# Optimization experiments

Hardware: AMD Instinct MI355X
Metric: run time of the kernel (lower is better)

Reference implementation:

```python
import jax, jax.numpy as jnp
import numpy as np

B, W, F, D, H, L = 8, 256, 16, 128, 8, 4
DH = D                      # dim_head = embedding_dims in the original call
INNER = H * DH              # 1024
TIME_EMB = 4
SCALE = DH ** -0.5


def causal_conv(x, w, b, dilation):
    # x: [B, F, W]; w: [F, 1, K] depthwise (groups=F); left-pad (K-1)*dilation -> causal
    k = w.shape[-1]
    pad = (k - 1) * dilation
    y = jax.lax.conv_general_dilated(
        x, w, window_strides=(1,), padding=[(pad, 0)], rhs_dilation=(dilation,),
        dimension_numbers=("NCH", "OIH", "NCH"), feature_group_count=F)
    return y + b[None, :, None]


def sinusoidal_pe(length, d):
    pos = jnp.arange(length, dtype=jnp.float32)[:, None]
    div = jnp.exp(jnp.arange(0, d, 2, dtype=jnp.float32) * (-np.log(10000.0) / d))
    pe = jnp.zeros((length, d), dtype=jnp.float32)
    pe = pe.at[:, 0::2].set(jnp.sin(pos * div)).at[:, 1::2].set(jnp.cos(pos * div))
    return pe  # [W, D]


def layer_norm(x, g, b):
    m = x.mean(-1, keepdims=True)
    v = x.var(-1, keepdims=True)
    return (x - m) * jax.lax.rsqrt(v + 1e-5) * g + b


def vt_attention(x, g, bln, wqkv, wout, bout):
    # x: [B, W, F, D] -> PreNorm then dual-axis (variable + temporal) attention
    h = layer_norm(x, g, bln)
    qkv = h @ wqkv                                   # [B,W,F,3*INNER]
    q, k, v = jnp.split(qkv, 3, axis=-1)
    heads = lambda t: t.reshape(B, W, F, H, DH)
    q, k, v = heads(q) * SCALE, heads(k), heads(v)
    # variable attention: attend across the feature axis (per time step)
    av = jax.nn.softmax(jnp.einsum("bwihe,bwjhe->bwhij", q, k), axis=-1)  # [B,W,H,F,F]
    ov = jnp.einsum("bwhij,bwjhe->bwihe", av, v)
    # temporal attention: attend across the window axis (per variable)
    at = jax.nn.softmax(jnp.einsum("bifhe,bjfhe->bfhij", q, k), axis=-1)  # [B,F,H,W,W]
    ot = jnp.einsum("bfhij,bjfhe->bifhe", at, v)
    o = (ov + ot).reshape(B, W, F, INNER)
    return o @ wout + bout                            # [B,W,F,D]


def setup_inputs() -> dict:
    key = jax.random.key(0)
    ks = jax.random.split(key, 16)
    n = lambda k, shape, sc: jax.random.normal(k, shape, dtype=jnp.float32) * sc
    return {
        "x": jax.random.normal(ks[0], (B, W, F), dtype=jnp.float32),
        "conv_w1": n(ks[1], (F, 1, 4), 0.3), "conv_b1": jnp.zeros((F,), jnp.float32),
        "conv_w2": n(ks[2], (F, 1, 8), 0.2), "conv_b2": jnp.zeros((F,), jnp.float32),
        "conv_w3": n(ks[3], (F, 1, 16), 0.15), "conv_b3": jnp.zeros((F,), jnp.float32),
        "w_val": n(ks[4], (TIME_EMB, D), 0.3), "b_val": jnp.zeros((D,), jnp.float32),
        "ln_g": jnp.ones((L, D), jnp.float32), "ln_b": jnp.zeros((L, D), jnp.float32),
        "w_qkv": n(ks[5], (L, D, 3 * INNER), D ** -0.5),
        "w_out": n(ks[6], (L, INNER, D), INNER ** -0.5),
        "b_out": jnp.zeros((L, D), jnp.float32),
        "w_head": n(ks[7], (F * D, F), (F * D) ** -0.5),
        "b_head": jnp.zeros((F,), jnp.float32),
    }


def reference(x, conv_w1, conv_b1, conv_w2, conv_b2, conv_w3, conv_b3,
              w_val, b_val, ln_g, ln_b, w_qkv, w_out, b_out, w_head, b_head):
    xt = jnp.transpose(x, (0, 2, 1))                  # b w f -> b f w
    c1 = causal_conv(xt, conv_w1, conv_b1, 1)
    c2 = causal_conv(xt, conv_w2, conv_b2, 2)
    c3 = causal_conv(xt, conv_w3, conv_b3, 3)
    s = jnp.stack([xt, c1, c2, c3], axis=-1)          # [B,F,W,4]
    s = jnp.transpose(s, (0, 2, 1, 3))                # [B,W,F,4]
    e = s @ w_val + b_val                             # [B,W,F,D]
    pe = sinusoidal_pe(W, D)                          # [W,D] broadcast over b,f
    h = e + pe[None, :, None, :]
    for l in range(L):
        xo = vt_attention(h, ln_g[l], ln_b[l], w_qkv[l], w_out[l], b_out[l])
        h = xo + h                                    # residual
    out = h.reshape(B, W, F * D) @ w_head + b_head    # [B,W,F]
    return out
```

## Files before the change

kernel.cpp:

```cpp
#include <hip/hip_runtime.h>
#include <hip/hip_bf16.h>
#include <math.h>

#define BB 8
#define WW 256
#define FF 16
#define DD 128
#define HH 8
#define NTOK (BB*WW*FF)
#define QSCALE 0.12751745f
#define INV_D (1.0f/128.0f)
#define LN10K_D 0.07195578415606394f

typedef __hip_bfloat16 bf16;
typedef short bf16x8 __attribute__((ext_vector_type(8)));
typedef float f32x4 __attribute__((ext_vector_type(4)));

__device__ __forceinline__ float bf2f(bf16 x){ return __bfloat162float(x); }
__device__ __forceinline__ bf16 f2bf(float x){ return __float2bfloat16(x); }
__device__ __forceinline__ unsigned short bfbits(float x){ bf16 b = f2bf(x); return *(unsigned short*)&b; }
__device__ __forceinline__ float bits2f(unsigned short u){ bf16 b = *(bf16*)&u; return __bfloat162float(b); }

#define MFMA16 __builtin_amdgcn_mfma_f32_16x16x32_bf16


__global__ __launch_bounds__(256) void prep_kernel(
    const float* __restrict__ wqkv, const float* __restrict__ wout,
    const float* __restrict__ wh,
    bf16* __restrict__ wqkvT, bf16* __restrict__ woutT, bf16* __restrict__ whT,
    const float* __restrict__ x,
    const float* __restrict__ w1, const float* __restrict__ b1,
    const float* __restrict__ w2, const float* __restrict__ b2,
    const float* __restrict__ w3, const float* __restrict__ b3,
    const float* __restrict__ wval, const float* __restrict__ bval,
    const float* __restrict__ g, const float* __restrict__ bln,
    float* __restrict__ h, bf16* __restrict__ hn)
{
    __shared__ __align__(16) char smem[16640];
    int tid = threadIdx.x;

    if (blockIdx.x < 544) {
        float (*tile)[65] = (float(*)[65])smem;
        int bx = blockIdx.x;
        const float* in; bf16* outp; int r0, c0, sin, sout, nmax;
        if (bx < 384) {
            int l = bx / 96, t = bx % 96;
            r0 = (t / 48)*64; c0 = (t % 48)*64;
            in = wqkv + (size_t)l*128*3072; outp = wqkvT + (size_t)l*3072*128;
            sin = 3072; sout = 128; nmax = 3072;
        } else if (bx < 512) {
            int j = bx - 384, l = j / 32, t = j % 32;
            r0 = (t / 2)*64; c0 = (t % 2)*64;
            in = wout + (size_t)l*1024*128; outp = woutT + (size_t)l*128*1024;
            sin = 128; sout = 1024; nmax = 128;
        } else {
            int t = bx - 512;
            r0 = t*64; c0 = 0;
            in = wh; outp = whT; sin = 16; sout = 2048; nmax = 16;
        }
        int rr = tid >> 2, cg = (tid & 3)*16;
        if (c0 + cg < nmax) {
            const float* src = in + (size_t)(r0 + rr)*sin + c0 + cg;
            #pragma unroll
            for (int i = 0; i < 4; i++)
                *(float4*)&tile[rr][cg + i*4] = *(const float4*)(src + i*4);
        }
        __syncthreads();
        int n = c0 + rr;
        if (n < nmax) {
            union { uint4 u[2]; unsigned short sh[16]; } o;
            #pragma unroll
            for (int e = 0; e < 16; e++) o.sh[e] = bfbits(tile[cg + e][rr]);
            bf16* dst = outp + (size_t)n*sout + r0 + cg;
            *(uint4*)dst = o.u[0];
            *(uint4*)(dst + 8) = o.u[1];
        }
        return;
    }

    float (*s)[4] = (float(*)[4])smem;
    float* hs = (float*)(smem + 256);
    int bw = blockIdx.x - 544;
    int b = bw >> 8, w = bw & 255;
    if (tid < 64) {
        int f = tid >> 2, t = tid & 3;
        const float* xb = x + (size_t)b*WW*FF + f;
        float v;
        if (t == 0) {
            v = xb[(size_t)w*FF];
        } else if (t == 1) {
            float acc = b1[f];
            #pragma unroll
            for (int kk = 0; kk < 4; kk++) { int t0 = w - (3-kk); if (t0 >= 0) acc += w1[f*4+kk]*xb[(size_t)t0*FF]; }
            v = acc;
        } else if (t == 2) {
            float acc = b2[f];
            #pragma unroll
            for (int kk = 0; kk < 8; kk++) { int t0 = w - (7-kk)*2; if (t0 >= 0) acc += w2[f*8+kk]*xb[(size_t)t0*FF]; }
            v = acc;
        } else {
            float acc = b3[f];
            #pragma unroll
            for (int kk = 0; kk < 16; kk++) { int t0 = w - (15-kk)*3; if (t0 >= 0) acc += w3[f*16+kk]*xb[(size_t)t0*FF]; }
            v = acc;
        }
        s[f][t] = v;
    }
    __syncthreads();
    #pragma unroll
    for (int r = 0; r < 8; r++) {
        int lin = r*256 + tid;
        int f = lin >> 7, d = lin & 127;
        float div = expf(-(float)(d & ~1) * LN10K_D);
        float arg = (float)w * div;
        float pe = (d & 1) ? cosf(arg) : sinf(arg);
        float e = bval[d] + pe;
        #pragma unroll
        for (int t = 0; t < 4; t++) e += s[f][t]*wval[t*128 + d];
        h[((size_t)bw*FF + f)*128 + d] = e;
        hs[f*132 + d] = e;
    }
    __syncthreads();
    int tok = tid >> 4, sub = tid & 15;
    float xv[8];
    #pragma unroll
    for (int e2 = 0; e2 < 8; e2++) xv[e2] = hs[tok*132 + sub*8 + e2];
    float s1 = 0.f, s2 = 0.f;
    #pragma unroll
    for (int e2 = 0; e2 < 8; e2++) { s1 += xv[e2]; s2 += xv[e2]*xv[e2]; }
    #pragma unroll
    for (int m = 1; m < 16; m <<= 1) { s1 += __shfl_xor(s1, m, 64); s2 += __shfl_xor(s2, m, 64); }
    float mean = s1*INV_D;
    float var  = s2*INV_D - mean*mean;
    float rs = rsqrtf(var + 1e-5f);
    union { uint4 u; unsigned short sh[8]; } ou;
    #pragma unroll
    for (int e2 = 0; e2 < 8; e2++) {
        int d = sub*8 + e2;
        ou.sh[e2] = bfbits((xv[e2]-mean)*rs*g[d] + bln[d]);
    }
    *(uint4*)(hn + ((size_t)bw*16 + tok)*128 + sub*8) = ou.u;
}

__global__ __launch_bounds__(256) void qkv_mfma(
    const bf16* __restrict__ hn, const bf16* __restrict__ wT,
    bf16* __restrict__ q, bf16* __restrict__ k, bf16* __restrict__ v)
{
    __shared__ __align__(16) unsigned short Cs[4][64][72];
    int tid = threadIdx.x;
    int lane = tid & 63, wave = tid >> 6;
    int quad = lane >> 4, l16 = lane & 15;
    int wm = wave >> 1, wn = wave & 1;
    int m0 = blockIdx.x * 128, n0 = blockIdx.y * 128;

    f32x4 acc[4][4];
    #pragma unroll
    for (int a = 0; a < 4; a++)
        #pragma unroll
        for (int c = 0; c < 4; c++) acc[a][c] = 0.f;

    #pragma unroll
    for (int kt = 0; kt < 4; kt++) {
        int ko = kt*32 + quad*8;
        bf16x8 af[4], bfr[4];
        #pragma unroll
        for (int tm = 0; tm < 4; tm++)
            af[tm] = *(const bf16x8*)(hn + (size_t)(m0 + wm*64 + tm*16 + l16)*128 + ko);
        #pragma unroll
        for (int tn = 0; tn < 4; tn++)
            bfr[tn] = *(const bf16x8*)(wT + (size_t)(n0 + wn*64 + tn*16 + l16)*128 + ko);
        #pragma unroll
        for (int tm = 0; tm < 4; tm++)
            #pragma unroll
            for (int tn = 0; tn < 4; tn++)
                acc[tm][tn] = MFMA16(af[tm], bfr[tn], acc[tm][tn], 0, 0, 0);
    }

    bf16* dst; int nrel; float scl; int isq;
    if (n0 < 1024)      { dst = q; nrel = n0;        scl = QSCALE; isq = 1; }
    else if (n0 < 2048) { dst = k; nrel = n0 - 1024; scl = 1.0f;   isq = 0; }
    else                { dst = v; nrel = n0 - 2048; scl = 1.0f;   isq = 0; }

    #pragma unroll
    for (int tm = 0; tm < 4; tm++)
        #pragma unroll
        for (int tn = 0; tn < 4; tn++)
            #pragma unroll
            for (int r = 0; r < 4; r++)
                Cs[wave][tm*16 + quad*4 + r][tn*16 + l16] = bfbits(acc[tm][tn][r]*scl);

    if (isq) {
        #pragma unroll
        for (int p = 0; p < 8; p++) {
            int row = p*8 + (lane >> 3);
            int c8  = (lane & 7)*8;
            uint4 val = *(const uint4*)&Cs[wave][row][c8];
            size_t gaddr = (size_t)(m0 + wm*64 + row)*1024 + nrel + wn*64 + c8;
            *(uint4*)(dst + gaddr) = val;
        }
    } else {
        int hh = nrel >> 7;
        #pragma unroll
        for (int p = 0; p < 8; p++) {
            int row = p*8 + (lane >> 3);
            int c8  = (lane & 7)*8;
            uint4 val = *(const uint4*)&Cs[wave][row][c8];
            int tok = m0 + wm*64 + row;
            int bl = tok >> 12, w = (tok >> 4) & 255, f = tok & 15;
            int d  = wn*64 + c8;
            size_t gaddr = ((size_t)((bl*16 + f)*8 + hh) << 15) + (size_t)w*128 + d;
            *(uint4*)(dst + gaddr) = val;
        }
    }
}

__global__ __launch_bounds__(256) void tattn_mfma(
    const bf16* __restrict__ q, const bf16* __restrict__ k, const bf16* __restrict__ v,
    bf16* __restrict__ o)
{
    __shared__ __align__(16) unsigned short Ks[64*136];
    __shared__ __align__(16) unsigned short VsT[128*72];
    __shared__ __align__(16) unsigned short Ps[4][16][72];
    unsigned short* Os = Ks;
    unsigned int* VsTdw = (unsigned int*)VsT;

    int bx = blockIdx.x;
    int hh = bx & 7, it2 = (bx>>3) & 1, f = (bx>>4) & 15, bl = bx >> 8;
    int tid = threadIdx.x;
    int lane = tid & 63, wave = tid >> 6;
    int quad = lane >> 4, l16 = lane & 15;

    size_t baseQ = ((size_t)(bl*WW)*FF + f)*1024 + (size_t)hh*128;
    size_t baseK = (size_t)((bl*16 + f)*8 + hh) << 15;

    #pragma unroll 1
    for (int pass = 0; pass < 2; pass++) {
        int i0 = it2*128 + pass*64;

        bf16x8 af[4];
        {
            size_t qa = baseQ + (size_t)(i0 + wave*16 + l16)*16384;
            #pragma unroll
            for (int kt = 0; kt < 4; kt++)
                af[kt] = *(const bf16x8*)(q + qa + kt*32 + quad*8);
        }

        f32x4 oacc[8];
        #pragma unroll
        for (int t = 0; t < 8; t++) oacc[t] = 0.f;
        float m_run[4], l_run[4];
        #pragma unroll
        for (int r = 0; r < 4; r++) { m_run[r] = -1e30f; l_run[r] = 0.f; }

        #pragma unroll 1
        for (int jt = 0; jt < 4; jt++) {
            __syncthreads();
            #pragma unroll
            for (int p4 = 0; p4 < 4; p4++) {
                int lin = p4*256 + tid;
                int row = lin >> 4, c8 = (lin & 15)*8;
                uint4 kv = *(const uint4*)(k + baseK + (size_t)(jt*64 + row)*128 + c8);
                *(uint4*)&Ks[row*136 + c8] = kv;
            }
            #pragma unroll
            for (int p = 0; p < 2; p++) {
                int lin = p*256 + tid;
                int j2 = lin & 31;
                int c2 = (lin >> 5)*8;
                union { uint4 u; unsigned short sh[8]; } a, b;
                a.u = *(const uint4*)(v + baseK + (size_t)(jt*64 + 2*j2)*128 + c2);
                b.u = *(const uint4*)(v + baseK + (size_t)(jt*64 + 2*j2 + 1)*128 + c2);
                int col2 = (((2*j2) + (c2 & 56)) & 63) >> 1;
                #pragma unroll
                for (int e = 0; e < 8; e++)
                    VsTdw[(c2+e)*36 + col2] = (unsigned int)a.sh[e] | ((unsigned int)b.sh[e] << 16);
            }
            __syncthreads();

            f32x4 st[4];
            #pragma unroll
            for (int t = 0; t < 4; t++) st[t] = 0.f;
            #pragma unroll
            for (int t = 0; t < 4; t++) {
                #pragma unroll
                for (int kt = 0; kt < 4; kt++) {
                    bf16x8 kf = *(const bf16x8*)&Ks[(t*16 + l16)*136 + kt*32 + quad*8];
                    st[t] = MFMA16(af[kt], kf, st[t], 0, 0, 0);
                }
            }

            float tmax[4];
            #pragma unroll
            for (int r = 0; r < 4; r++) tmax[r] = fmaxf(fmaxf(st[0][r], st[1][r]), fmaxf(st[2][r], st[3][r]));
            #pragma unroll
            for (int m = 1; m < 16; m <<= 1)
                #pragma unroll
                for (int r = 0; r < 4; r++) tmax[r] = fmaxf(tmax[r], __shfl_xor(tmax[r], m, 64));
            float alpha[4], rsum[4];
            #pragma unroll
            for (int r = 0; r < 4; r++) {
                float mnew = fmaxf(m_run[r], tmax[r]);
                alpha[r] = exp2f(m_run[r] - mnew);
                m_run[r] = mnew;
                rsum[r] = 0.f;
            }
            #pragma unroll
            for (int t = 0; t < 4; t++)
                #pragma unroll
                for (int r = 0; r < 4; r++) {
                    float pp = exp2f(st[t][r] - m_run[r]);
                    st[t][r] = pp;
                    rsum[r] += pp;
                }
            #pragma unroll
            for (int m = 1; m < 16; m <<= 1)
                #pragma unroll
                for (int r = 0; r < 4; r++) rsum[r] += __shfl_xor(rsum[r], m, 64);
            #pragma unroll
            for (int r = 0; r < 4; r++) l_run[r] = l_run[r]*alpha[r] + rsum[r];
            #pragma unroll
            for (int t = 0; t < 8; t++)
                #pragma unroll
                for (int r = 0; r < 4; r++) oacc[t][r] *= alpha[r];

            #pragma unroll
            for (int t = 0; t < 4; t++)
                #pragma unroll
                for (int r = 0; r < 4; r++)
                    Ps[wave][quad*4+r][t*16+l16] = bfbits(st[t][r]);

            #pragma unroll
            for (int kt2 = 0; kt2 < 2; kt2++) {
                int kbase = kt2*32 + quad*8;
                bf16x8 pf = *(const bf16x8*)&Ps[wave][l16][kbase];
                #pragma unroll
                for (int t = 0; t < 8; t++) {
                    int d = t*16 + l16;
                    int colstart = (kbase + (((d>>3)&7) << 3)) & 63;
                    bf16x8 vf = *(const bf16x8*)&VsT[d*72 + colstart];
                    oacc[t] = MFMA16(pf, vf, oacc[t], 0, 0, 0);
                }
            }
        }

        __syncthreads();
        float inv[4];
        #pragma unroll
        for (int r = 0; r < 4; r++) inv[r] = 1.f / l_run[r];
        #pragma unroll
        for (int t = 0; t < 8; t++)
            #pragma unroll
            for (int r = 0; r < 4; r++)
                Os[(wave*16 + quad*4 + r)*136 + t*16 + l16] = bfbits(oacc[t][r]*inv[r]);
        __syncthreads();
        #pragma unroll
        for (int r4 = 0; r4 < 4; r4++) {
            int row = r4*4 + quad;
            uint4 val = *(const uint4*)&Os[(wave*16 + row)*136 + l16*8];
            size_t gaddr = baseQ + (size_t)(i0 + wave*16 + row)*16384 + l16*8;
            *(uint4*)(o + gaddr) = val;
        }
    }
}

__global__ __launch_bounds__(256) void vproj_mfma(
    const bf16* __restrict__ q, const bf16* __restrict__ k, const bf16* __restrict__ v,
    const bf16* __restrict__ ot, const bf16* __restrict__ woT,
    const float* __restrict__ bo, float* __restrict__ h,
    bf16* __restrict__ hn, const float* __restrict__ gN, const float* __restrict__ bN,
    int donorm, int tokbase)
{
    __shared__ __align__(16) unsigned short VsT[16768];
    __shared__ __align__(16) unsigned short Ps[4][16][24];
    __shared__ float red2[4][16][2];
    unsigned short* Osum = VsT;
    unsigned int* VsTdw = (unsigned int*)VsT;

    int tid = threadIdx.x;
    int lane = tid & 63, wave = tid >> 6, quad = lane >> 4, l16 = lane & 15;
    int bl = blockIdx.x >> 8, w = blockIdx.x & 255;
    size_t base = (size_t)blockIdx.x * 16384;
    size_t woff = (size_t)w * 128;

    uint4 otpre[8];
    #pragma unroll
    for (int u = 0; u < 8; u++) {
        int lin = u*256 + tid;
        int fr = lin >> 7, dc = (lin & 127)*8;
        otpre[u] = *(const uint4*)(ot + base + (size_t)fr*1024 + dc);
    }

    #pragma unroll
    for (int p = 0; p < 4; p++) {
        int lin = p*256 + tid;
        int j2 = lin & 7;
        int d0 = (lin >> 3)*8;
        int hh2 = d0 >> 7, dd = d0 & 127;
        union { uint4 u; unsigned short sh[8]; } a, b;
        a.u = *(const uint4*)(v + (((size_t)((bl*16 + 2*j2  )*8 + hh2)) << 15) + woff + dd);
        b.u = *(const uint4*)(v + (((size_t)((bl*16 + 2*j2+1)*8 + hh2)) << 15) + woff + dd);
        #pragma unroll
        for (int e = 0; e < 8; e++)
            VsTdw[(d0+e)*8 + j2] = (unsigned int)a.sh[e] | ((unsigned int)b.sh[e] << 16);
    }
    __syncthreads();

    bf16x8 zf = {0,0,0,0,0,0,0,0};
    f32x4 oa[2][8];
    #pragma unroll
    for (int hi = 0; hi < 2; hi++) {
        int hh = wave*2 + hi;
        size_t hb = base + hh*128;

        f32x4 s = {0.f,0.f,0.f,0.f};
        size_t ka = (((size_t)((bl*16 + l16)*8 + hh)) << 15) + woff;
        #pragma unroll
        for (int kt = 0; kt < 4; kt++) {
            bf16x8 qf = *(const bf16x8*)(q + hb + (size_t)l16*1024 + kt*32 + quad*8);
            bf16x8 kf = *(const bf16x8*)(k + ka + kt*32 + quad*8);
            s = MFMA16(qf, kf, s, 0, 0, 0);
        }
        float p[4];
        #pragma unroll
        for (int r = 0; r < 4; r++) {
            float mxv = s[r];
            #pragma unroll
            for (int m = 1; m < 16; m <<= 1) mxv = fmaxf(mxv, __shfl_xor(mxv, m, 64));
            float e = exp2f(s[r] - mxv);
            float smv = e;
            #pragma unroll
            for (int m = 1; m < 16; m <<= 1) smv += __shfl_xor(smv, m, 64);
            p[r] = e / smv;
        }
        #pragma unroll
        for (int r = 0; r < 4; r++) Ps[wave][quad*4+r][l16] = bfbits(p[r]);

        bf16x8 pf = zf;
        if (quad < 2) pf = *(const bf16x8*)&Ps[wave][l16][quad*8];
        #pragma unroll
        for (int dt = 0; dt < 8; dt++) oa[hi][dt] = 0.f;
        #pragma unroll
        for (int dt = 0; dt < 8; dt++) {
            bf16x8 vf = zf;
            if (quad < 2) vf = *(const bf16x8*)&VsT[(size_t)(hh*128 + dt*16 + l16)*16 + quad*8];
            oa[hi][dt] = MFMA16(pf, vf, oa[hi][dt], 0, 0, 0);
        }
    }

    __syncthreads();
    #pragma unroll
    for (int hi = 0; hi < 2; hi++) {
        int hh = wave*2 + hi;
        #pragma unroll
        for (int dt = 0; dt < 8; dt++)
            #pragma unroll
            for (int r = 0; r < 4; r++)
                Osum[(quad*4 + r)*1048 + hh*128 + dt*16 + l16] = bfbits(oa[hi][dt][r]);
    }
    __syncthreads();

    #pragma unroll
    for (int u = 0; u < 8; u++) {
        int lin = u*256 + tid;
        int fr = lin >> 7, dc = (lin & 127)*8;
        union { uint4 u4; unsigned short sh[8]; } a, bsh, wv;
        a.u4   = otpre[u];
        bsh.u4 = *(const uint4*)&Osum[fr*1048 + dc];
        #pragma unroll
        for (int e = 0; e < 8; e++)
            wv.sh[e] = bfbits(bits2f(a.sh[e]) + bits2f(bsh.sh[e]));
        *(uint4*)&Osum[fr*1048 + dc] = wv.u4;
    }
    __syncthreads();

    f32x4 pacc[2];
    pacc[0] = 0.f; pacc[1] = 0.f;
    #pragma unroll 4
    for (int kt2 = 0; kt2 < 32; kt2++) {
        bf16x8 af2 = *(const bf16x8*)&Osum[l16*1048 + kt2*32 + quad*8];
        #pragma unroll
        for (int nt = 0; nt < 2; nt++) {
            bf16x8 bfr = *(const bf16x8*)(woT + (size_t)(wave*32 + nt*16 + l16)*1024 + kt2*32 + quad*8);
            pacc[nt] = MFMA16(af2, bfr, pacc[nt], 0, 0, 0);
        }
    }

    int htok = tokbase + blockIdx.x*16;
    float hv[2][4];
    #pragma unroll
    for (int nt = 0; nt < 2; nt++) {
        int n = wave*32 + nt*16 + l16;
        float bias = bo[n];
        #pragma unroll
        for (int r = 0; r < 4; r++) {
            size_t idx = (size_t)(htok + quad*4 + r)*128 + n;
            float nv = h[idx] + pacc[nt][r] + bias;
            h[idx] = nv;
            hv[nt][r] = nv;
        }
    }

    if (donorm) {
        float s1[4], s2[4];
        #pragma unroll
        for (int r = 0; r < 4; r++) {
            s1[r] = hv[0][r] + hv[1][r];
            s2[r] = hv[0][r]*hv[0][r] + hv[1][r]*hv[1][r];
        }
        #pragma unroll
        for (int m = 1; m < 16; m <<= 1)
            #pragma unroll
            for (int r = 0; r < 4; r++) {
                s1[r] += __shfl_xor(s1[r], m, 64);
                s2[r] += __shfl_xor(s2[r], m, 64);
            }
        __syncthreads();
        if (l16 == 0) {
            #pragma unroll
            for (int r = 0; r < 4; r++) {
                red2[wave][quad*4+r][0] = s1[r];
                red2[wave][quad*4+r][1] = s2[r];
            }
        }
        __syncthreads();
        #pragma unroll
        for (int nt = 0; nt < 2; nt++) {
            int n = wave*32 + nt*16 + l16;
            float gn = gN[n], bn = bN[n];
            #pragma unroll
            for (int r = 0; r < 4; r++) {
                int t = quad*4 + r;
                float t1 = red2[0][t][0] + red2[1][t][0] + red2[2][t][0] + red2[3][t][0];
                float t2 = red2[0][t][1] + red2[1][t][1] + red2[2][t][1] + red2[3][t][1];
                float mean = t1*INV_D;
                float var  = t2*INV_D - mean*mean;
                float rsv = rsqrtf(var + 1e-5f);
                Osum[t*1048 + n] = bfbits((hv[nt][r]-mean)*rsv*gn + bn);
            }
        }
        __syncthreads();
        int row = tid >> 4, c8 = (tid & 15)*8;
        uint4 val = *(const uint4*)&Osum[row*1048 + c8];
        *(uint4*)(hn + (size_t)(htok + row)*128 + c8) = val;
    }
}

__global__ __launch_bounds__(256) void head_mfma(
    const float* __restrict__ h, const bf16* __restrict__ whT,
    const float* __restrict__ bh, float* __restrict__ out)
{
    __shared__ float sred[4][16][17];
    int tid = threadIdx.x;
    int lane = tid & 63, wave = tid >> 6, quad = lane >> 4, l16 = lane & 15;
    int bw0 = blockIdx.x * 16;
    const float* hrow = h + (size_t)(bw0 + l16)*2048 + wave*512;
    const bf16* wrow  = whT + (size_t)l16*2048 + wave*512;

    f32x4 acc = {0.f,0.f,0.f,0.f};
    #pragma unroll 4
    for (int kc = 0; kc < 16; kc++) {
        int ko = kc*32 + quad*8;
        float4 a0 = *(const float4*)(hrow + ko);
        float4 a1 = *(const float4*)(hrow + ko + 4);
        union { bf16x8 v; unsigned short sh[8]; } ua;
        ua.sh[0]=bfbits(a0.x); ua.sh[1]=bfbits(a0.y); ua.sh[2]=bfbits(a0.z); ua.sh[3]=bfbits(a0.w);
        ua.sh[4]=bfbits(a1.x); ua.sh[5]=bfbits(a1.y); ua.sh[6]=bfbits(a1.z); ua.sh[7]=bfbits(a1.w);
        bf16x8 bv = *(const bf16x8*)(wrow + ko);
        acc = MFMA16(ua.v, bv, acc, 0, 0, 0);
    }
    #pragma unroll
    for (int r = 0; r < 4; r++) sred[wave][quad*4+r][l16] = acc[r];
    __syncthreads();
    int i = tid >> 4, n = tid & 15;
    float s = bh[n] + sred[0][i][n] + sred[1][i][n] + sred[2][i][n] + sred[3][i][n];
    out[(size_t)(bw0 + i)*16 + n] = s;
}

extern "C" void kernel_launch(void* const* d_in, const int* in_sizes, int n_in,
                              void* d_out, int out_size, void* d_ws, size_t ws_size,
                              hipStream_t stream)
{
    const float* x    = (const float*)d_in[0];
    const float* w1   = (const float*)d_in[1];
    const float* b1   = (const float*)d_in[2];
    const float* w2   = (const float*)d_in[3];
    const float* b2   = (const float*)d_in[4];
    const float* w3   = (const float*)d_in[5];
    const float* b3   = (const float*)d_in[6];
    const float* wval = (const float*)d_in[7];
    const float* bval = (const float*)d_in[8];
    const float* lng  = (const float*)d_in[9];
    const float* lnb  = (const float*)d_in[10];
    const float* wqkv = (const float*)d_in[11];
    const float* wout = (const float*)d_in[12];
    const float* bout = (const float*)d_in[13];
    const float* wh   = (const float*)d_in[14];
    const float* bh   = (const float*)d_in[15];
    float* out = (float*)d_out;

    char* ws = (char*)d_ws;
    bf16*  wqkvT = (bf16*)ws;
    bf16*  woutT = (bf16*)(ws + 3145728);
    bf16*  whT   = (bf16*)(ws + 4194304);
    float* h     = (float*)(ws + 4259840);
    bf16*  hn    = (bf16*)(ws + 21037056);
    const size_t qoff = 29425664ull;

    int NBL = 1;
    if      (ws_size >= qoff + 8ull*4ull*8388608ull) NBL = 8;
    else if (ws_size >= qoff + 4ull*4ull*8388608ull) NBL = 4;
    else if (ws_size >= qoff + 2ull*4ull*8388608ull) NBL = 2;
    size_t bsz = (size_t)NBL * 8388608ull;
    bf16* q  = (bf16*)(ws + qoff);
    bf16* kk = (bf16*)(ws + qoff + bsz);
    bf16* vv = (bf16*)(ws + qoff + 2*bsz);
    bf16* oo = (bf16*)(ws + qoff + 3*bsz);

    prep_kernel<<<544 + BB*WW, 256, 0, stream>>>(
        wqkv, wout, wh, wqkvT, woutT, whT,
        x, w1,b1, w2,b2, w3,b3, wval, bval, lng, lnb, h, hn);

    for (int l = 0; l < 4; l++) {
        const bf16* wqT_l = wqkvT + (size_t)l*3072*128;
        const bf16* woT_l = woutT + (size_t)l*128*1024;
        const float* bo_l = bout + l*128;
        int donorm = (l < 3) ? 1 : 0;
        const float* gN = lng + (donorm ? (l+1)*128 : 0);
        const float* bN = lnb + (donorm ? (l+1)*128 : 0);
        for (int bb = 0; bb < BB; bb += NBL) {
            int tokbase = bb*WW*FF;
            qkv_mfma<<<dim3(NBL*32, 24), 256, 0, stream>>>(
                hn + (size_t)tokbase*128, wqT_l, q, kk, vv);
            tattn_mfma<<<NBL*FF*HH*2, 256, 0, stream>>>(q, kk, vv, oo);
            vproj_mfma<<<NBL*WW, 256, 0, stream>>>(q, kk, vv, oo, woT_l,
                                                   bo_l, h, hn, gN, bN,
                                                   donorm, tokbase);
        }
    }

    head_mfma<<<BB*WW/16, 256, 0, stream>>>(h, whT, bh, out);
}
```

Baseline: 1.447 ms.

## Split temporal attention blocks per 64-row tile, prefetch K/V into registers, hoist vproj loads

```diff
diff --git a/kernel.cpp b/kernel.cpp
--- a/kernel.cpp
+++ b/kernel.cpp
@@ -225,7 +225,8 @@
     unsigned int* VsTdw = (unsigned int*)VsT;
 
     int bx = blockIdx.x;
-    int hh = bx & 7, it2 = (bx>>3) & 1, f = (bx>>4) & 15, bl = bx >> 8;
+    int hh = bx & 7, it = (bx>>3) & 3, f = (bx>>5) & 15, bl = bx >> 9;
+    int i0 = it*64;
     int tid = threadIdx.x;
     int lane = tid & 63, wave = tid >> 6;
     int quad = lane >> 4, l16 = lane & 15;
@@ -233,133 +234,148 @@
     size_t baseQ = ((size_t)(bl*WW)*FF + f)*1024 + (size_t)hh*128;
     size_t baseK = (size_t)((bl*16 + f)*8 + hh) << 15;
 
+    bf16x8 af[4];
+    {
+        size_t qa = baseQ + (size_t)(i0 + wave*16 + l16)*16384;
+        #pragma unroll
+        for (int kt = 0; kt < 4; kt++)
+            af[kt] = *(const bf16x8*)(q + qa + kt*32 + quad*8);
+    }
+
+    f32x4 oacc[8];
+    #pragma unroll
+    for (int t = 0; t < 8; t++) oacc[t] = 0.f;
+    float m_run[4], l_run[4];
+    #pragma unroll
+    for (int r = 0; r < 4; r++) { m_run[r] = -1e30f; l_run[r] = 0.f; }
+
+    int krow = tid >> 4, kc8 = (tid & 15)*8;
+    int vj2 = tid & 31, vc2 = (tid >> 5)*8;
+
+    uint4 kld[4]; uint4 vla[2], vlb[2];
+    #pragma unroll
+    for (int p4 = 0; p4 < 4; p4++)
+        kld[p4] = *(const uint4*)(k + baseK + (size_t)(p4*16 + krow)*128 + kc8);
+    #pragma unroll
+    for (int p = 0; p < 2; p++) {
+        int j2 = vj2, c2 = p*128 + vc2;
+        j2 = (p*256 + tid) & 31; c2 = ((p*256 + tid) >> 5)*8;
+        vla[p] = *(const uint4*)(v + baseK + (size_t)(2*j2)*128 + c2);
+        vlb[p] = *(const uint4*)(v + baseK + (size_t)(2*j2 + 1)*128 + c2);
+    }
+
     #pragma unroll 1
-    for (int pass = 0; pass < 2; pass++) {
-        int i0 = it2*128 + pass*64;
-
-        bf16x8 af[4];
-        {
-            size_t qa = baseQ + (size_t)(i0 + wave*16 + l16)*16384;
-            #pragma unroll
-            for (int kt = 0; kt < 4; kt++)
-                af[kt] = *(const bf16x8*)(q + qa + kt*32 + quad*8);
-        }
-
-        f32x4 oacc[8];
-        #pragma unroll
-        for (int t = 0; t < 8; t++) oacc[t] = 0.f;
-        float m_run[4], l_run[4];
-        #pragma unroll
-        for (int r = 0; r < 4; r++) { m_run[r] = -1e30f; l_run[r] = 0.f; }
-
-        #pragma unroll 1
-        for (int jt = 0; jt < 4; jt++) {
-            __syncthreads();
-            #pragma unroll
-            for (int p4 = 0; p4 < 4; p4++) {
-                int lin = p4*256 + tid;
-                int row = lin >> 4, c8 = (lin & 15)*8;
-                uint4 kv = *(const uint4*)(k + baseK + (size_t)(jt*64 + row)*128 + c8);
-                *(uint4*)&Ks[row*136 + c8] = kv;
+    for (int jt = 0; jt < 4; jt++) {
+        __syncthreads();
+        #pragma unroll
+        for (int p4 = 0; p4 < 4; p4++)
+            *(uint4*)&Ks[(p4*16 + krow)*136 + kc8] = kld[p4];
+        #pragma unroll
+        for (int p = 0; p < 2; p++) {
+            int j2 = (p*256 + tid) & 31, c2 = ((p*256 + tid) >> 5)*8;
+            union { uint4 u; unsigned short sh[8]; } a, b;
+            a.u = vla[p]; b.u = vlb[p];
+            int col2 = (((2*j2) + (c2 & 56)) & 63) >> 1;
+            #pragma unroll
+            for (int e = 0; e < 8; e++)
+                VsTdw[(c2+e)*36 + col2] = (unsigned int)a.sh[e] | ((unsigned int)b.sh[e] << 16);
+        }
+        if (jt < 3) {
+            int jn = jt + 1;
+            #pragma unroll
+            for (int p4 = 0; p4 < 4; p4++)
+                kld[p4] = *(const uint4*)(k + baseK + (size_t)(jn*64 + p4*16 + krow)*128 + kc8);
+            #pragma unroll
+            for (int p = 0; p < 2; p++) {
+                int j2 = (p*256 + tid) & 31, c2 = ((p*256 + tid) >> 5)*8;
+                vla[p] = *(const uint4*)(v + baseK + (size_t)(jn*64 + 2*j2)*128 + c2);
+                vlb[p] = *(const uint4*)(v + baseK + (size_t)(jn*64 + 2*j2 + 1)*128 + c2);
             }
-            #pragma unroll
-            for (int p = 0; p < 2; p++) {
-                int lin = p*256 + tid;
-                int j2 = lin & 31;
-                int c2 = (lin >> 5)*8;
-                union { uint4 u; unsigned short sh[8]; } a, b;
-                a.u = *(const uint4*)(v + baseK + (size_t)(jt*64 + 2*j2)*128 + c2);
-                b.u = *(const uint4*)(v + baseK + (size_t)(jt*64 + 2*j2 + 1)*128 + c2);
-                int col2 = (((2*j2) + (c2 & 56)) & 63) >> 1;
-                #pragma unroll
-                for (int e = 0; e < 8; e++)
-                    VsTdw[(c2+e)*36 + col2] = (unsigned int)a.sh[e] | ((unsigned int)b.sh[e] << 16);
+        }
+        __syncthreads();
+
+        f32x4 st[4];
+        #pragma unroll
+        for (int t = 0; t < 4; t++) st[t] = 0.f;
+        #pragma unroll
+        for (int t = 0; t < 4; t++) {
+            #pragma unroll
+            for (int kt = 0; kt < 4; kt++) {
+                bf16x8 kf = *(const bf16x8*)&Ks[(t*16 + l16)*136 + kt*32 + quad*8];
+                st[t] = MFMA16(af[kt], kf, st[t], 0, 0, 0);
             }
-            __syncthreads();
-
-            f32x4 st[4];
-            #pragma unroll
-            for (int t = 0; t < 4; t++) st[t] = 0.f;
-            #pragma unroll
-            for (int t = 0; t < 4; t++) {
-                #pragma unroll
-                for (int kt = 0; kt < 4; kt++) {
-                    bf16x8 kf = *(const bf16x8*)&Ks[(t*16 + l16)*136 + kt*32 + quad*8];
-                    st[t] = MFMA16(af[kt], kf, st[t], 0, 0, 0);
-                }
+        }
+
+        float tmax[4];
+        #pragma unroll
+        for (int r = 0; r < 4; r++) tmax[r] = fmaxf(fmaxf(st[0][r], st[1][r]), fmaxf(st[2][r], st[3][r]));
+        #pragma unroll
+        for (int m = 1; m < 16; m <<= 1)
+            #pragma unroll
+            for (int r = 0; r < 4; r++) tmax[r] = fmaxf(tmax[r], __shfl_xor(tmax[r], m, 64));
+        float alpha[4], rsum[4];
+        #pragma unroll
+        for (int r = 0; r < 4; r++) {
+            float mnew = fmaxf(m_run[r], tmax[r]);
+            alpha[r] = exp2f(m_run[r] - mnew);
+            m_run[r] = mnew;
+            rsum[r] = 0.f;
+        }
+        #pragma unroll
+        for (int t = 0; t < 4; t++)
+            #pragma unroll
+            for (int r = 0; r < 4; r++) {
+                float pp = exp2f(st[t][r] - m_run[r]);
+                st[t][r] = pp;
+                rsum[r] += pp;
             }
-
-            float tmax[4];
-            #pragma unroll
-            for (int r = 0; r < 4; r++) tmax[r] = fmaxf(fmaxf(st[0][r], st[1][r]), fmaxf(st[2][r], st[3][r]));
-            #pragma unroll
-            for (int m = 1; m < 16; m <<= 1)
-                #pragma unroll
-                for (int r = 0; r < 4; r++) tmax[r] = fmaxf(tmax[r], __shfl_xor(tmax[r], m, 64));
-            float alpha[4], rsum[4];
-            #pragma unroll
-            for (int r = 0; r < 4; r++) {
-                float mnew = fmaxf(m_run[r], tmax[r]);
-                alpha[r] = exp2f(m_run[r] - mnew);
-                m_run[r] = mnew;
-                rsum[r] = 0.f;
+        #pragma unroll
+        for (int m = 1; m < 16; m <<= 1)
+            #pragma unroll
+            for (int r = 0; r < 4; r++) rsum[r] += __shfl_xor(rsum[r], m, 64);
+        #pragma unroll
+        for (int r = 0; r < 4; r++) l_run[r] = l_run[r]*alpha[r] + rsum[r];
+        #pragma unroll
+        for (int t = 0; t < 8; t++)
+            #pragma unroll
+            for (int r = 0; r < 4; r++) oacc[t][r] *= alpha[r];
+
+        #pragma unroll
+        for (int t = 0; t < 4; t++)
+            #pragma unroll
+            for (int r = 0; r < 4; r++)
+                Ps[wave][quad*4+r][t*16+l16] = bfbits(st[t][r]);
+
+        #pragma unroll
+        for (int kt2 = 0; kt2 < 2; kt2++) {
+            int kbase = kt2*32 + quad*8;
+            bf16x8 pf = *(const bf16x8*)&Ps[wave][l16][kbase];
+            #pragma unroll
+            for (int t = 0; t < 8; t++) {
+                int d = t*16 + l16;
+                int colstart = (kbase + (((d>>3)&7) << 3)) & 63;
+                bf16x8 vf = *(const bf16x8*)&VsT[d*72 + colstart];
+                oacc[t] = MFMA16(pf, vf, oacc[t], 0, 0, 0);
             }
-            #pragma unroll
-            for (int t = 0; t < 4; t++)
-                #pragma unroll
-                for (int r = 0; r < 4; r++) {
-                    float pp = exp2f(st[t][r] - m_run[r]);
-                    st[t][r] = pp;
-                    rsum[r] += pp;
-                }
-            #pragma unroll
-            for (int m = 1; m < 16; m <<= 1)
-                #pragma unroll
-                for (int r = 0; r < 4; r++) rsum[r] += __shfl_xor(rsum[r], m, 64);
-            #pragma unroll
-            for (int r = 0; r < 4; r++) l_run[r] = l_run[r]*alpha[r] + rsum[r];
-            #pragma unroll
-            for (int t = 0; t < 8; t++)
-                #pragma unroll
-                for (int r = 0; r < 4; r++) oacc[t][r] *= alpha[r];
-
-            #pragma unroll
-            for (int t = 0; t < 4; t++)
-                #pragma unroll
-                for (int r = 0; r < 4; r++)
-                    Ps[wave][quad*4+r][t*16+l16] = bfbits(st[t][r]);
-
-            #pragma unroll
-            for (int kt2 = 0; kt2 < 2; kt2++) {
-                int kbase = kt2*32 + quad*8;
-                bf16x8 pf = *(const bf16x8*)&Ps[wave][l16][kbase];
-                #pragma unroll
-                for (int t = 0; t < 8; t++) {
-                    int d = t*16 + l16;
-                    int colstart = (kbase + (((d>>3)&7) << 3)) & 63;
-                    bf16x8 vf = *(const bf16x8*)&VsT[d*72 + colstart];
-                    oacc[t] = MFMA16(pf, vf, oacc[t], 0, 0, 0);
-                }
-            }
-        }
-
-        __syncthreads();
-        float inv[4];
-        #pragma unroll
-        for (int r = 0; r < 4; r++) inv[r] = 1.f / l_run[r];
-        #pragma unroll
-        for (int t = 0; t < 8; t++)
-            #pragma unroll
-            for (int r = 0; r < 4; r++)
-                Os[(wave*16 + quad*4 + r)*136 + t*16 + l16] = bfbits(oacc[t][r]*inv[r]);
-        __syncthreads();
-        #pragma unroll
-        for (int r4 = 0; r4 < 4; r4++) {
-            int row = r4*4 + quad;
-            uint4 val = *(const uint4*)&Os[(wave*16 + row)*136 + l16*8];
-            size_t gaddr = baseQ + (size_t)(i0 + wave*16 + row)*16384 + l16*8;
-            *(uint4*)(o + gaddr) = val;
-        }
+        }
+    }
+
+    __syncthreads();
+    float inv[4];
+    #pragma unroll
+    for (int r = 0; r < 4; r++) inv[r] = 1.f / l_run[r];
+    #pragma unroll
+    for (int t = 0; t < 8; t++)
+        #pragma unroll
+        for (int r = 0; r < 4; r++)
+            Os[(wave*16 + quad*4 + r)*136 + t*16 + l16] = bfbits(oacc[t][r]*inv[r]);
+    __syncthreads();
+    #pragma unroll
+    for (int r4 = 0; r4 < 4; r4++) {
+        int row = r4*4 + quad;
+        uint4 val = *(const uint4*)&Os[(wave*16 + row)*136 + l16*8];
+        size_t gaddr = baseQ + (size_t)(i0 + wave*16 + row)*16384 + l16*8;
+        *(uint4*)(o + gaddr) = val;
     }
 }
 
@@ -382,6 +398,19 @@
     size_t base = (size_t)blockIdx.x * 16384;
     size_t woff = (size_t)w * 128;
 
+    bf16x8 qpre[2][4], kpre[2][4];
+    #pragma unroll
+    for (int hi = 0; hi < 2; hi++) {
+        int hh = wave*2 + hi;
+        size_t hb = base + hh*128 + (size_t)l16*1024;
+        size_t ka = (((size_t)((bl*16 + l16)*8 + hh)) << 15) + woff;
+        #pragma unroll
+        for (int kt = 0; kt < 4; kt++) {
+            qpre[hi][kt] = *(const bf16x8*)(q + hb + kt*32 + quad*8);
+            kpre[hi][kt] = *(const bf16x8*)(k + ka + kt*32 + quad*8);
+        }
+    }
+
     uint4 otpre[8];
     #pragma unroll
     for (int u = 0; u < 8; u++) {
@@ -410,16 +439,11 @@
     #pragma unroll
     for (int hi = 0; hi < 2; hi++) {
         int hh = wave*2 + hi;
-        size_t hb = base + hh*128;
 
         f32x4 s = {0.f,0.f,0.f,0.f};
-        size_t ka = (((size_t)((bl*16 + l16)*8 + hh)) << 15) + woff;
-        #pragma unroll
-        for (int kt = 0; kt < 4; kt++) {
-            bf16x8 qf = *(const bf16x8*)(q + hb + (size_t)l16*1024 + kt*32 + quad*8);
-            bf16x8 kf = *(const bf16x8*)(k + ka + kt*32 + quad*8);
-            s = MFMA16(qf, kf, s, 0, 0, 0);
-        }
+        #pragma unroll
+        for (int kt = 0; kt < 4; kt++)
+            s = MFMA16(qpre[hi][kt], kpre[hi][kt], s, 0, 0, 0);
         float p[4];
         #pragma unroll
         for (int r = 0; r < 4; r++) {
@@ -631,7 +655,7 @@
             int tokbase = bb*WW*FF;
             qkv_mfma<<<dim3(NBL*32, 24), 256, 0, stream>>>(
                 hn + (size_t)tokbase*128, wqT_l, q, kk, vv);
-            tattn_mfma<<<NBL*FF*HH*2, 256, 0, stream>>>(q, kk, vv, oo);
+            tattn_mfma<<<NBL*FF*HH*4, 256, 0, stream>>>(q, kk, vv, oo);
             vproj_mfma<<<NBL*WW, 256, 0, stream>>>(q, kk, vv, oo, woT_l,
                                                    bo_l, h, hn, gN, bN,
                                                    donorm, tokbase);
```

Result: slower. 1.496 ms (+3.4%).
